# Optimization experiments

Hardware: AMD Instinct MI355X
Metric: run time of the kernel (lower is better)

## Reference

```python
import jax, jax.numpy as jnp
import numpy as np

B, S, N = 64, 32, 128            # batch, seq_len, padded nodes per graph
DV, DW, DH = 512, 300, 1024      # dim_v, dim_word, dim_hidden
CLS, T_CTRL, L = 1024, 12, 4     # cls_fc_dim, controller steps, stack_len
NQ, NA, NE, NATTR, M = 100, 28, 16, 1000, 6  # vocabs, edge cats, attrs, num modules
# module order: 0 NoOp, 1 Find(push), 2 Transform, 3 Filter, 4 And, 5 Describe

def _valid_mat():
    m = np.zeros((L, M), dtype=np.float32)
    for s in range(L):
        m[s, 0] = 1.0
        m[s, 1] = 1.0 if s < L - 1 else 0.0
        m[s, 2] = 1.0 if s >= 1 else 0.0
        m[s, 3] = 1.0 if s >= 1 else 0.0
        m[s, 4] = 1.0 if s >= 2 else 0.0
        m[s, 5] = 1.0 if s >= 1 else 0.0
    return jnp.asarray(m)

VALID_MAT = _valid_mat()

def setup_inputs() -> dict:
    key = jax.random.key(0)
    ks = jax.random.split(key, 24)
    nrm = lambda k, sh, sc: jax.random.normal(k, sh, jnp.float32) * sc
    inp = {}
    inp['questions'] = jax.random.randint(ks[0], (B, S), 0, NQ)
    inp['questions_len'] = jax.random.randint(ks[1], (B,), 8, S + 1)
    inp['conn'] = (jax.random.uniform(ks[2], (B, N, N)) < 0.2).astype(jnp.float32)
    inp['cat_mat'] = jax.random.randint(ks[3], (B, N, N), 0, NE)
    inp['v_idx'] = jax.random.randint(ks[4], (B, N), 0, NATTR)
    inp['attr_emb'] = nrm(ks[5], (NATTR, DV), 1.0 / np.sqrt(DV))
    inp['edge_cat_vectors'] = nrm(ks[6], (NE, DV), 1.0 / np.sqrt(DV))
    inp['enc_emb'] = nrm(ks[7], (NQ, DW), 1.0 / np.sqrt(DW))
    inp['Wx'] = nrm(ks[8], (DW, 4 * DH), 1.0 / np.sqrt(DW))
    inp['Wh'] = nrm(ks[9], (DH, 4 * DH), 1.0 / np.sqrt(DH))
    inp['b_lstm'] = jnp.zeros((4 * DH,), jnp.float32)
    inp['W_cq'] = nrm(ks[10], (2 * DH, DH), 1.0 / np.sqrt(2 * DH))
    inp['b_cq'] = jnp.zeros((DH,), jnp.float32)
    inp['W_mod'] = nrm(ks[11], (DH, M), 1.0 / np.sqrt(DH))
    inp['W_att'] = nrm(ks[12], (DH, DH), 1.0 / np.sqrt(DH))
    inp['W_q'] = nrm(ks[13], (DH, DV), np.sqrt(2.0 / DH))
    inp['b_q'] = jnp.zeros((DV,), jnp.float32)
    inp['W_find'] = nrm(ks[14], (DV, DV), 1.0 / np.sqrt(DV))
    inp['W_desc'] = nrm(ks[15], (DV, DV), 1.0 / np.sqrt(DV))
    inp['W_cls1'] = nrm(ks[16], (DV + DH, CLS), np.sqrt(2.0 / (DV + DH)))
    inp['b_cls1'] = jnp.zeros((CLS,), jnp.float32)
    inp['W_cls2'] = nrm(ks[17], (CLS, NA), np.sqrt(2.0 / CLS))
    inp['b_cls2'] = jnp.zeros((NA,), jnp.float32)
    return inp

def _read(st, p):
    return jnp.einsum('bnl,bl->bn', st, p)

def _write(st, p, a):
    pe = p[:, None, :]
    return a[:, :, None] * pe + st * (1.0 - pe)

def _ptr_fw(p):
    q = jnp.concatenate([jnp.zeros_like(p[:, :1]), p[:, :-1]], axis=1)
    return q.at[:, -1].add(p[:, -1])

def _ptr_bw(p):
    q = jnp.concatenate([p[:, 1:], jnp.zeros_like(p[:, :1])], axis=1)
    return q.at[:, 0].add(p[:, 0])

def reference(questions, questions_len, conn, cat_mat, v_idx, attr_emb,
              edge_cat_vectors, enc_emb, Wx, Wh, b_lstm, W_cq, b_cq, W_mod,
              W_att, W_q, b_q, W_find, W_desc, W_cls1, b_cls1, W_cls2, b_cls2):
    # ---- question encoder: embedding + LSTM over time-major sequence ----
    emb = enc_emb[questions].transpose(1, 0, 2)  # [S,B,DW]

    def lstm_step(carry, x):
        h, c = carry
        g = x @ Wx + h @ Wh + b_lstm
        i, f, gg, o = jnp.split(g, 4, axis=-1)
        c = jax.nn.sigmoid(f) * c + jax.nn.sigmoid(i) * jnp.tanh(gg)
        h = jax.nn.sigmoid(o) * jnp.tanh(c)
        return (h, c), h

    init = (jnp.zeros((B, DH), jnp.float32), jnp.zeros((B, DH), jnp.float32))
    _, outs = jax.lax.scan(lstm_step, init, emb)            # [S,B,DH]
    outs_b = outs.transpose(1, 0, 2)                         # [B,S,DH]
    q_hidden = outs_b[jnp.arange(B), questions_len - 1]      # last valid state

    mask = jnp.arange(S)[:, None] < questions_len[None, :]   # [S,B]
    feat = attr_emb[v_idx]                                   # [B,N,DV]
    bidx = jnp.arange(B)[:, None, None]

    att_stack = jnp.zeros((B, N, L), jnp.float32)
    stack_ptr = jnp.zeros((B, L), jnp.float32).at[:, 0].set(1.0)
    mem = jnp.zeros((B, DV), jnp.float32)
    c_ctrl = jnp.zeros((B, DH), jnp.float32)
    inv_sqrt_dv = 1.0 / np.sqrt(DV)

    for t in range(T_CTRL):
        # ---- controller step: module distribution + textual attention ----
        cq = jnp.tanh(jnp.concatenate([c_ctrl, q_hidden], axis=1) @ W_cq + b_cq)
        module_prob = jax.nn.softmax(cq @ W_mod, axis=-1)     # [B,M]
        al = jnp.einsum('sbh,bh->sb', outs, cq @ W_att)
        cv = jax.nn.softmax(jnp.where(mask, al, -1e9), axis=0)
        c_ctrl = jnp.einsum('sb,sbh->bh', cv, outs)
        c_i = jax.nn.relu(c_ctrl @ W_q + b_q)                 # [B,DV]

        # ---- validity masking of module distribution ----
        validity = jnp.round(stack_ptr @ VALID_MAT)           # [B,M]
        mp = module_prob * validity
        s = jnp.sum(mp, axis=1, keepdims=True)
        mp = mp / jnp.where(s > 0, s, 1.0)

        # ---- run every module, soft-average by module prob ----
        a_find = jax.nn.sigmoid(jnp.einsum('bnd,bd->bn', feat @ W_find, c_i) * inv_sqrt_dv)
        a_in = _read(att_stack, stack_ptr)
        # Transform: edge-category-weighted message passing on graph
        we = jax.nn.softmax(c_i @ edge_cat_vectors.T, axis=-1)   # [B,NE]
        ew = we[bidx, cat_mat] * conn                            # [B,N,N]
        a_trans = jnp.minimum(jnp.einsum('bij,bj->bi', ew, a_in), 1.0)
        p_fw = _ptr_fw(stack_ptr)
        p_bw = _ptr_bw(stack_ptr)
        a_prev = _read(att_stack, p_bw)
        pooled = jnp.einsum('bn,bnd->bd', a_in, feat) / (jnp.sum(a_in, 1, keepdims=True) + 1e-6)
        res = [
            (att_stack, stack_ptr, mem),                                  # NoOp
            (_write(att_stack, p_fw, a_find), p_fw, mem),                 # Find (push)
            (_write(att_stack, stack_ptr, a_trans), stack_ptr, mem),      # Transform
            (_write(att_stack, stack_ptr, a_in * a_find), stack_ptr, mem),# Filter
            (_write(att_stack, p_bw, jnp.minimum(a_prev, a_in)), p_bw, mem),  # And (pop)
            (att_stack, p_bw, pooled @ W_desc),                           # Describe
        ]
        att_stack = jnp.einsum('bm,mbnl->bnl', mp, jnp.stack([r[0] for r in res]))
        stack_ptr = jnp.einsum('bm,mbl->bl', mp, jnp.stack([r[1] for r in res]))
        mem = jnp.einsum('bm,mbd->bd', mp, jnp.stack([r[2] for r in res]))

    final = jnp.concatenate([mem, q_hidden], axis=1)
    h1 = jax.nn.relu(final @ W_cls1 + b_cls1)
    logits = h1 @ W_cls2 + b_cls2
    return logits
```

## Files before the change

kernel.cpp:

```cpp
#include <hip/hip_runtime.h>
#include <math.h>

#define B 64
#define S 32
#define NN 128
#define DV 512
#define DW 300
#define DH 1024
#define CLS 1024
#define T_CTRL 12
#define LL 4
#define NA 28
#define NE 16
#define MM 6

__device__ __forceinline__ float sigmoidf_(float x) { return 1.0f / (1.0f + expf(-x)); }

template<bool TRANS, class AF, class WF>
__device__ __forceinline__ void gemm_core(int kbeg, int Kc, AF loadA, WF loadW,
                                          float* part, int Cld, int orow) {
  __shared__ float Ast[2][64 * 36];
  __shared__ float Ws[2][32 * 64];
  const int tid = threadIdx.x;
  const int j0 = blockIdx.x * 64;
  const int ntiles = Kc >> 5;
  const int rg = tid & 15, cg = tid >> 4;
  float4 av[2], wv[2];

  auto fetch = [&](int kt) {
    #pragma unroll
    for (int i2 = 0; i2 < 2; ++i2) {
      int idx = tid + i2 * 256;
      av[i2] = loadA(idx >> 3, kt + (idx & 7) * 4);
    }
    #pragma unroll
    for (int i2 = 0; i2 < 2; ++i2) {
      int idx = tid + i2 * 256;
      if (!TRANS) wv[i2] = loadW(kt + (idx >> 4), j0 + (idx & 15) * 4);
      else        wv[i2] = loadW(j0 + (idx >> 3), kt + (idx & 7) * 4);
    }
  };
  auto commit = [&](int buf) {
    #pragma unroll
    for (int i2 = 0; i2 < 2; ++i2) {
      int idx = tid + i2 * 256;
      *(float4*)&Ast[buf][(idx >> 3) * 36 + (idx & 7) * 4] = av[i2];
    }
    #pragma unroll
    for (int i2 = 0; i2 < 2; ++i2) {
      int idx = tid + i2 * 256;
      if (!TRANS) {
        *(float4*)&Ws[buf][(idx >> 4) * 64 + (idx & 15) * 4] = wv[i2];
      } else {
        int jloc = idx >> 3, k4 = (idx & 7) * 4;
        Ws[buf][(k4 + 0) * 64 + jloc] = wv[i2].x;
        Ws[buf][(k4 + 1) * 64 + jloc] = wv[i2].y;
        Ws[buf][(k4 + 2) * 64 + jloc] = wv[i2].z;
        Ws[buf][(k4 + 3) * 64 + jloc] = wv[i2].w;
      }
    }
  };

  float acc[4][4] = {};
  fetch(kbeg);
  commit(0);
  __syncthreads();
  for (int i = 0; i < ntiles; ++i) {
    if (i + 1 < ntiles) fetch(kbeg + (i + 1) * 32);
    const float* As = &Ast[i & 1][0];
    const float* Wp = &Ws[i & 1][0];
    #pragma unroll
    for (int kq = 0; kq < 8; ++kq) {
      float4 a0 = *(const float4*)&As[(rg     ) * 36 + kq * 4];
      float4 a1 = *(const float4*)&As[(rg + 16) * 36 + kq * 4];
      float4 a2 = *(const float4*)&As[(rg + 32) * 36 + kq * 4];
      float4 a3 = *(const float4*)&As[(rg + 48) * 36 + kq * 4];
      float4 w0 = *(const float4*)&Wp[(kq * 4 + 0) * 64 + cg * 4];
      float4 w1 = *(const float4*)&Wp[(kq * 4 + 1) * 64 + cg * 4];
      float4 w2 = *(const float4*)&Wp[(kq * 4 + 2) * 64 + cg * 4];
      float4 w3 = *(const float4*)&Wp[(kq * 4 + 3) * 64 + cg * 4];
      #define STEP(m, AV) \
        acc[m][0]=fmaf(AV.x,w0.x,acc[m][0]); acc[m][1]=fmaf(AV.x,w0.y,acc[m][1]); \
        acc[m][2]=fmaf(AV.x,w0.z,acc[m][2]); acc[m][3]=fmaf(AV.x,w0.w,acc[m][3]); \
        acc[m][0]=fmaf(AV.y,w1.x,acc[m][0]); acc[m][1]=fmaf(AV.y,w1.y,acc[m][1]); \
        acc[m][2]=fmaf(AV.y,w1.z,acc[m][2]); acc[m][3]=fmaf(AV.y,w1.w,acc[m][3]); \
        acc[m][0]=fmaf(AV.z,w2.x,acc[m][0]); acc[m][1]=fmaf(AV.z,w2.y,acc[m][1]); \
        acc[m][2]=fmaf(AV.z,w2.z,acc[m][2]); acc[m][3]=fmaf(AV.z,w2.w,acc[m][3]); \
        acc[m][0]=fmaf(AV.w,w3.x,acc[m][0]); acc[m][1]=fmaf(AV.w,w3.y,acc[m][1]); \
        acc[m][2]=fmaf(AV.w,w3.z,acc[m][2]); acc[m][3]=fmaf(AV.w,w3.w,acc[m][3]);
      STEP(0, a0) STEP(1, a1) STEP(2, a2) STEP(3, a3)
      #undef STEP
    }
    if (i + 1 < ntiles) { __syncthreads(); commit((i + 1) & 1); __syncthreads(); }
  }
  float* op = part + (size_t)orow * 64 * Cld + j0 + cg * 4;
  #pragma unroll
  for (int m = 0; m < 4; ++m)
    *(float4*)&op[(size_t)(rg + 16 * m) * Cld] = make_float4(acc[m][0], acc[m][1], acc[m][2], acc[m][3]);
}

__global__ void init_kernel(float* c_lstm, float* c_ctrl, float* att_stack, float* mem, float* sptr) {
  int idx = blockIdx.x * 256 + threadIdx.x;
  if (idx < B * DH) { c_lstm[idx] = 0.f; c_ctrl[idx] = 0.f; }
  if (idx < B * NN * LL) att_stack[idx] = 0.f;
  if (idx < B * DV) mem[idx] = 0.f;
  if (idx < B * LL) sptr[idx] = ((idx & (LL - 1)) == 0) ? 1.f : 0.f;
}

__global__ void embq_kernel(const int* __restrict__ questions, const float* __restrict__ enc_emb,
                            float* __restrict__ embq) {
  int row = blockIdx.x;
  int t = row >> 6, b = row & 63;
  int qid = questions[b * S + t];
  int c = threadIdx.x;
  embq[(size_t)row * 320 + c] = (c < DW) ? enc_emb[(size_t)qid * DW + c] : 0.f;
}

__global__ __launch_bounds__(256) void xgemm_kernel(const float* __restrict__ embq,
                                                    const float* __restrict__ Wx,
                                                    float* __restrict__ X) {
  auto Al = [&](int r, int k) -> float4 {
    return *(const float4*)&embq[(size_t)(blockIdx.y * 64 + r) * 320 + k];
  };
  auto Wl = [&](int k, int j) -> float4 {
    if (k < 300) return *(const float4*)&Wx[(size_t)k * 4096 + j];
    return make_float4(0.f, 0.f, 0.f, 0.f);
  };
  gemm_core<false>(0, 320, Al, Wl, X, 4096, blockIdx.y);
}

__global__ __launch_bounds__(256) void f2_kernel(const float* __restrict__ attr_emb,
                                                 const float* __restrict__ W_find,
                                                 float* __restrict__ F2) {
  auto Al = [&](int r, int k) -> float4 {
    int gr = blockIdx.y * 64 + r;
    if (gr > 999) gr = 999;
    return *(const float4*)&attr_emb[(size_t)gr * 512 + k];
  };
  auto Wl = [&](int k, int j) -> float4 { return *(const float4*)&W_find[(size_t)k * 512 + j]; };
  gemm_core<false>(0, 512, Al, Wl, F2, 512, blockIdx.y);
}

__global__ __launch_bounds__(256) void lstm_gemm_kernel(const float* __restrict__ h_prev,
                                                        const float* __restrict__ Wh,
                                                        float* __restrict__ part) {
  auto Al = [&](int r, int k) -> float4 { return *(const float4*)&h_prev[(size_t)r * 1024 + k]; };
  auto Wl = [&](int k, int j) -> float4 { return *(const float4*)&Wh[(size_t)k * 4096 + j]; };
  gemm_core<false>(blockIdx.y * 128, 128, Al, Wl, part, 4096, blockIdx.y);
}

__global__ __launch_bounds__(256) void lstm_gate_kernel(const float* __restrict__ part, int SK,
                                                        const float* __restrict__ X, int t,
                                                        const float* __restrict__ b_lstm,
                                                        float* __restrict__ h_out, float* __restrict__ c_st) {
  int idx = blockIdx.x * 256 + threadIdx.x;
  int b = idx >> 10, j = idx & 1023;
  const float* xr = X + ((size_t)t * 64 + b) * 4096;
  float gi = xr[j], gf = xr[1024 + j], gg = xr[2048 + j], go = xr[3072 + j];
  const float* pb = part + (size_t)b * 4096;
  for (int c = 0; c < SK; ++c) {
    const float* p = pb + (size_t)c * 262144;
    gi += p[j]; gf += p[1024 + j]; gg += p[2048 + j]; go += p[3072 + j];
  }
  gi += b_lstm[j]; gf += b_lstm[1024 + j]; gg += b_lstm[2048 + j]; go += b_lstm[3072 + j];
  float c = sigmoidf_(gf) * c_st[idx] + sigmoidf_(gi) * tanhf(gg);
  h_out[idx] = sigmoidf_(go) * tanhf(c);
  c_st[idx] = c;
}

__global__ __launch_bounds__(256) void c1_kernel(const float* __restrict__ c_ctrl,
                                                 const float* __restrict__ outs, const int* __restrict__ qlen,
                                                 const float* __restrict__ W_cq, float* __restrict__ partA,
                                                 const float* __restrict__ partE, const float* __restrict__ mp,
                                                 float* __restrict__ mem, int do_epi) {
  if (blockIdx.x == 16) {
    if (!do_epi) return;
    int t0 = blockIdx.y * 256 + threadIdx.x;
    #pragma unroll
    for (int i = 0; i < 4; ++i) {
      int f4 = t0 + i * 2048;
      int b = f4 >> 7, j = (f4 & 127) * 4;
      const float* m = &mp[b * 6];
      float s04 = m[0] + m[1] + m[2] + m[3] + m[4];
      float4 s = make_float4(0.f, 0.f, 0.f, 0.f);
      for (int c = 0; c < 8; ++c) {
        float4 v = *(const float4*)&partE[(size_t)c * 32768 + b * 512 + j];
        s.x += v.x; s.y += v.y; s.z += v.z; s.w += v.w;
      }
      float4 o = *(const float4*)&mem[b * 512 + j];
      o.x = s04 * o.x + m[5] * s.x; o.y = s04 * o.y + m[5] * s.y;
      o.z = s04 * o.z + m[5] * s.z; o.w = s04 * o.w + m[5] * s.w;
      *(float4*)&mem[b * 512 + j] = o;
    }
    return;
  }
  auto Al = [&](int r, int k) -> float4 {
    if (k < 1024) return *(const float4*)&c_ctrl[r * 1024 + k];
    int tq = qlen[r] - 1;
    return *(const float4*)&outs[(size_t)tq * 65536 + r * 1024 + (k - 1024)];
  };
  auto Wl = [&](int k, int j) -> float4 { return *(const float4*)&W_cq[(size_t)k * 1024 + j]; };
  gemm_core<false>(blockIdx.y * 256, 256, Al, Wl, partA, 1024, blockIdx.y);
}

__global__ __launch_bounds__(256) void c2_kernel(const float* __restrict__ partA,
                                                 const float* __restrict__ b_cq,
                                                 const float* __restrict__ W_att,
                                                 const float* __restrict__ W_mod,
                                                 float* __restrict__ partB) {
  auto Al = [&](int r, int k) -> float4 {
    float4 s = *(const float4*)&b_cq[k];
    for (int c = 0; c < 8; ++c) {
      float4 v = *(const float4*)&partA[(size_t)c * 65536 + r * 1024 + k];
      s.x += v.x; s.y += v.y; s.z += v.z; s.w += v.w;
    }
    return make_float4(tanhf(s.x), tanhf(s.y), tanhf(s.z), tanhf(s.w));
  };
  auto Wl = [&](int k, int j) -> float4 {
    if (j < 1024) return *(const float4*)&W_att[(size_t)k * 1024 + j];
    float v[4];
    #pragma unroll
    for (int i = 0; i < 4; ++i) {
      int jj = j + i;
      v[i] = (jj < 1030) ? W_mod[(size_t)k * 6 + (jj - 1024)] : 0.f;
    }
    return make_float4(v[0], v[1], v[2], v[3]);
  };
  gemm_core<false>(blockIdx.y * 64, 64, Al, Wl, partB, 1088, blockIdx.y);
}

__global__ __launch_bounds__(256) void attn_kernel(const float* __restrict__ partB,
                                                   const float* __restrict__ outs,
                                                   const int* __restrict__ qlen,
                                                   float* __restrict__ c_ctrl) {
  int b = blockIdx.x >> 2, hq = blockIdx.x & 3;
  int tid = threadIdx.x;
  __shared__ float aw[DH];
  __shared__ float alv[S];
  __shared__ float cvs[S];
  {
    int c4 = tid * 4;
    float4 s = make_float4(0.f, 0.f, 0.f, 0.f);
    for (int c = 0; c < 16; ++c) {
      float4 v = *(const float4*)&partB[(size_t)c * 69632 + b * 1088 + c4];
      s.x += v.x; s.y += v.y; s.z += v.z; s.w += v.w;
    }
    *(float4*)&aw[c4] = s;
  }
  __syncthreads();
  {
    int wv = tid >> 6, lane = tid & 63;
    #pragma unroll
    for (int u = 0; u < 4; ++u) {
      int s2 = wv * 4 + u;
      const float4* orow = (const float4*)&outs[(size_t)s2 * 65536 + b * 1024];
      float pr = 0.f;
      #pragma unroll
      for (int q = 0; q < 4; ++q) {
        float4 f = orow[lane + 64 * q];
        float4 w = *(const float4*)&aw[(lane + 64 * q) * 4];
        pr += f.x * w.x + f.y * w.y + f.z * w.z + f.w * w.w;
      }
      #pragma unroll
      for (int off = 32; off > 0; off >>= 1) pr += __shfl_xor(pr, off);
      if (lane == 0) alv[s2] = pr;
    }
  }
  __syncthreads();
  if (tid < 64) {
    int len = qlen[b];
    float v = (tid < S && tid < len) ? alv[tid] : -1e9f;
    float mx = v;
    #pragma unroll
    for (int off = 32; off > 0; off >>= 1) mx = fmaxf(mx, __shfl_xor(mx, off));
    float e = (tid < S && tid < len) ? expf(v - mx) : 0.f;
    float sm = e;
    #pragma unroll
    for (int off = 32; off > 0; off >>= 1) sm += __shfl_xor(sm, off);
    if (tid < S) cvs[tid] = e / sm;
  }
  __syncthreads();
  {
    int h = hq * 256 + tid;
    float a = 0.f;
    #pragma unroll 8
    for (int s2 = 0; s2 < S; ++s2)
      a = fmaf(cvs[s2], outs[(size_t)s2 * 65536 + b * 1024 + h], a);
    c_ctrl[b * 1024 + h] = a;
  }
}

__global__ __launch_bounds__(256) void c4_kernel(const float* __restrict__ c_ctrl,
                                                 const float* __restrict__ W_q,
                                                 float* __restrict__ partC) {
  auto Al = [&](int r, int k) -> float4 { return *(const float4*)&c_ctrl[r * 1024 + k]; };
  auto Wl = [&](int k, int j) -> float4 { return *(const float4*)&W_q[(size_t)k * 512 + j]; };
  gemm_core<false>(blockIdx.y * 64, 64, Al, Wl, partC, 512, blockIdx.y);
}

__global__ __launch_bounds__(256) void prep_kernel(const float* __restrict__ partC,
                                                   const float* __restrict__ partB,
                                                   const float* __restrict__ b_q,
                                                   const float* __restrict__ edge_cat,
                                                   const float* __restrict__ sptr_in,
                                                   const float* __restrict__ att_stack,
                                                   float* __restrict__ c_i, float* __restrict__ we,
                                                   float* __restrict__ mp, float* __restrict__ spv,
                                                   float* __restrict__ ain, float* __restrict__ aw4,
                                                   float* __restrict__ asum) {
  int b = blockIdx.x, tid = threadIdx.x;
  __shared__ float ci[512];
  __shared__ float lds[64];
  for (int col = tid; col < 512; col += 256) {
    float s = b_q[col];
    for (int c = 0; c < 16; ++c) s += partC[(size_t)c * 32768 + b * 512 + col];
    s = fmaxf(s, 0.f);
    ci[col] = s;
    c_i[b * 512 + col] = s;
  }
  if (tid < MM) {
    float s = 0.f;
    for (int c = 0; c < 16; ++c) s += partB[(size_t)c * 69632 + b * 1088 + 1024 + tid];
    lds[16 + tid] = s;
  }
  __syncthreads();
  {
    int wv = tid >> 6, lane = tid & 63;
    for (int e = wv; e < NE; e += 4) {
      const float* er = &edge_cat[(size_t)e * 512];
      float p = 0.f;
      #pragma unroll
      for (int q = 0; q < 8; ++q) p = fmaf(ci[lane + 64 * q], er[lane + 64 * q], p);
      #pragma unroll
      for (int off = 32; off > 0; off >>= 1) p += __shfl_xor(p, off);
      if (lane == 0) lds[e] = p;
    }
  }
  __syncthreads();
  if (tid == 0) {
    float mx = lds[0];
    for (int e = 1; e < NE; ++e) mx = fmaxf(mx, lds[e]);
    float sm = 0.f, ex[NE];
    for (int e = 0; e < NE; ++e) { ex[e] = expf(lds[e] - mx); sm += ex[e]; }
    for (int e = 0; e < NE; ++e) we[b * NE + e] = ex[e] / sm;
    float mx2 = lds[16];
    for (int m = 1; m < MM; ++m) mx2 = fmaxf(mx2, lds[16 + m]);
    float e6[MM], sm2 = 0.f;
    for (int m = 0; m < MM; ++m) { e6[m] = expf(lds[16 + m] - mx2); sm2 += e6[m]; }
    float p0 = sptr_in[b * 4 + 0], p1 = sptr_in[b * 4 + 1];
    float p2 = sptr_in[b * 4 + 2], p3 = sptr_in[b * 4 + 3];
    float sp[12];
    sp[0] = p0; sp[1] = p1; sp[2] = p2; sp[3] = p3;
    sp[4] = 0.f;      sp[5] = p0; sp[6] = p1; sp[7] = p2 + p3;
    sp[8] = p0 + p1;  sp[9] = p2; sp[10] = p3; sp[11] = 0.f;
    for (int i = 0; i < 12; ++i) { spv[b * 12 + i] = sp[i]; lds[22 + i] = sp[i]; }
    float val[MM];
    val[0] = rintf(p0 + p1 + p2 + p3);
    val[1] = rintf(p0 + p1 + p2);
    val[2] = rintf(p1 + p2 + p3);
    val[3] = val[2];
    val[4] = rintf(p2 + p3);
    val[5] = val[2];
    float mpv[MM], ssum = 0.f;
    #pragma unroll
    for (int m = 0; m < MM; ++m) { mpv[m] = (e6[m] / sm2) * val[m]; ssum += mpv[m]; }
    float inv = (ssum > 0.f) ? 1.f / ssum : 1.f;
    #pragma unroll
    for (int m = 0; m < MM; ++m) mp[b * MM + m] = mpv[m] * inv;
  }
  __syncthreads();
  if (tid < 128) {
    float4 st = *(const float4*)&att_stack[(b * NN + tid) * LL];
    float ainv = st.x * lds[22] + st.y * lds[23] + st.z * lds[24] + st.w * lds[25];
    float ap   = st.x * lds[30] + st.y * lds[31] + st.z * lds[32] + st.w * lds[33];
    ain[b * NN + tid] = ainv;
    aw4[b * NN + tid] = fminf(ap, ainv);
    float t2 = ainv;
    #pragma unroll
    for (int off = 32; off > 0; off >>= 1) t2 += __shfl_xor(t2, off);
    if ((tid & 63) == 0) lds[40 + (tid >> 6)] = t2;
  }
  __syncthreads();
  if (tid == 0) asum[b] = lds[40] + lds[41] + 1e-6f;
}

__global__ __launch_bounds__(256) void stackf_kernel(const int* __restrict__ v_idx,
                                                     const float* __restrict__ attr_emb,
                                                     const float* __restrict__ F2,
                                                     const float* __restrict__ c_i,
                                                     const float* __restrict__ we,
                                                     const int* __restrict__ cat_mat,
                                                     const float* __restrict__ conn,
                                                     const float* __restrict__ ain,
                                                     const float* __restrict__ asum,
                                                     float* __restrict__ afind,
                                                     float* __restrict__ atr,
                                                     float* __restrict__ pooled) {
  int job = blockIdx.x, tid = threadIdx.x;
  __shared__ float lds[192];
  if (job < 2048) {
    int gw = job * 4 + (tid >> 6);
    int b = gw >> 7, n = gw & 127, lane = tid & 63;
    int vid = v_idx[b * NN + n];
    const float4* fp = (const float4*)&F2[(size_t)vid * DV];
    const float4* up = (const float4*)&c_i[(size_t)b * DV];
    float pr = 0.f;
    #pragma unroll
    for (int q = 0; q < 2; ++q) {
      float4 f = fp[lane + 64 * q], u = up[lane + 64 * q];
      pr += f.x * u.x + f.y * u.y + f.z * u.z + f.w * u.w;
    }
    #pragma unroll
    for (int off = 32; off > 0; off >>= 1) pr += __shfl_xor(pr, off);
    if (lane == 0) afind[b * NN + n] = sigmoidf_(pr * 0.04419417382415922f);
  } else if (job < 2560) {
    int j2 = job - 2048;
    int b = j2 >> 3, ig = j2 & 7;
    if (tid < 128) lds[tid] = ain[b * NN + tid];
    else if (tid < 144) lds[tid] = we[b * NE + tid - 128];
    __syncthreads();
    int i = ig * 16 + (tid >> 4);
    const int* crow = &cat_mat[((size_t)b * NN + i) * NN];
    const float* nrow = &conn[((size_t)b * NN + i) * NN];
    float a = 0.f;
    #pragma unroll
    for (int q = 0; q < 8; ++q) {
      int j = (tid & 15) + 16 * q;
      a = fmaf(lds[128 + crow[j]] * nrow[j], lds[j], a);
    }
    a += __shfl_xor(a, 1); a += __shfl_xor(a, 2); a += __shfl_xor(a, 4); a += __shfl_xor(a, 8);
    if ((tid & 15) == 0) atr[b * NN + i] = fminf(a, 1.f);
  } else {
    int j3 = job - 2560;
    int b = j3 >> 1, d = (j3 & 1) * 256 + tid;
    int* vidL = (int*)&lds[128];
    if (tid < 128) { lds[tid] = ain[b * NN + tid]; vidL[tid] = v_idx[b * NN + tid]; }
    __syncthreads();
    float a = 0.f;
    #pragma unroll 4
    for (int n = 0; n < NN; ++n)
      a = fmaf(lds[n], attr_emb[(size_t)vidL[n] * DV + d], a);
    pooled[b * DV + d] = a / asum[b];
  }
}

__global__ __launch_bounds__(256) void c7u_kernel(const float* __restrict__ pooled,
                                                  const float* __restrict__ W_desc,
                                                  float* __restrict__ partE,
                                                  const float* __restrict__ spv,
                                                  const float* __restrict__ mp,
                                                  const float* __restrict__ afind,
                                                  const float* __restrict__ ain,
                                                  const float* __restrict__ atr,
                                                  const float* __restrict__ aw4,
                                                  float* __restrict__ att_stack,
                                                  float* __restrict__ sptr) {
  int tid = threadIdx.x;
  if (blockIdx.y < 8) {
    auto Al = [&](int r, int k) -> float4 { return *(const float4*)&pooled[r * 512 + k]; };
    auto Wl = [&](int k, int j) -> float4 { return *(const float4*)&W_desc[(size_t)k * 512 + j]; };
    gemm_core<false>(blockIdx.y * 64, 64, Al, Wl, partE, 512, blockIdx.y);
    return;
  }
  int b = (blockIdx.y - 8) * 8 + blockIdx.x;
  __shared__ float sp[12], smp[MM];
  if (tid < 12) sp[tid] = spv[b * 12 + tid];
  else if (tid < 12 + MM) smp[tid - 12] = mp[b * MM + (tid - 12)];
  __syncthreads();
  #pragma unroll
  for (int i = 0; i < 2; ++i) {
    int e = tid + i * 256;
    int n = e >> 2, l = e & 3;
    float st = att_stack[(b * NN + n) * LL + l];
    float keep = smp[0] + smp[5] + smp[1] * (1.f - sp[4 + l]) + (smp[2] + smp[3]) * (1.f - sp[l])
               + smp[4] * (1.f - sp[8 + l]);
    float add = sp[4 + l] * smp[1] * afind[b * NN + n]
              + sp[l] * (smp[2] * atr[b * NN + n] + smp[3] * ain[b * NN + n] * afind[b * NN + n])
              + sp[8 + l] * smp[4] * aw4[b * NN + n];
    att_stack[(b * NN + n) * LL + l] = keep * st + add;
  }
  if (tid < LL)
    sptr[b * LL + tid] = (smp[0] + smp[2] + smp[3]) * sp[tid] + smp[1] * sp[4 + tid]
                       + (smp[4] + smp[5]) * sp[8 + tid];
}

__global__ __launch_bounds__(256) void cl1_kernel(const float* __restrict__ partE,
                                                  const float* __restrict__ mp,
                                                  const float* __restrict__ mem,
                                                  const float* __restrict__ outs,
                                                  const int* __restrict__ qlen,
                                                  const float* __restrict__ W_cls1,
                                                  float* __restrict__ partH) {
  auto Al = [&](int r, int k) -> float4 {
    if (k < 512) {
      float4 s = make_float4(0.f, 0.f, 0.f, 0.f);
      for (int c = 0; c < 8; ++c) {
        float4 v = *(const float4*)&partE[(size_t)c * 32768 + r * 512 + k];
        s.x += v.x; s.y += v.y; s.z += v.z; s.w += v.w;
      }
      const float* m = &mp[r * 6];
      float s04 = m[0] + m[1] + m[2] + m[3] + m[4];
      float4 o = *(const float4*)&mem[r * 512 + k];
      return make_float4(s04 * o.x + m[5] * s.x, s04 * o.y + m[5] * s.y,
                         s04 * o.z + m[5] * s.z, s04 * o.w + m[5] * s.w);
    }
    int tq = qlen[r] - 1;
    return *(const float4*)&outs[(size_t)tq * 65536 + r * 1024 + (k - 512)];
  };
  auto Wl = [&](int k, int j) -> float4 { return *(const float4*)&W_cls1[(size_t)k * 1024 + j]; };
  gemm_core<false>(blockIdx.y * 192, 192, Al, Wl, partH, 1024, blockIdx.y);
}

__global__ __launch_bounds__(256) void cl2_kernel(const float* __restrict__ partH,
                                                  const float* __restrict__ b_cls1,
                                                  const float* __restrict__ W_cls2,
                                                  float* __restrict__ partJ) {
  auto Al = [&](int r, int k) -> float4 {
    float4 s = *(const float4*)&b_cls1[k];
    for (int c = 0; c < 8; ++c) {
      float4 v = *(const float4*)&partH[(size_t)c * 65536 + r * 1024 + k];
      s.x += v.x; s.y += v.y; s.z += v.z; s.w += v.w;
    }
    return make_float4(fmaxf(s.x, 0.f), fmaxf(s.y, 0.f), fmaxf(s.z, 0.f), fmaxf(s.w, 0.f));
  };
  auto Wl = [&](int k, int j) -> float4 {
    float v[4];
    #pragma unroll
    for (int i = 0; i < 4; ++i) { int jj = j + i; v[i] = (jj < NA) ? W_cls2[(size_t)k * NA + jj] : 0.f; }
    return make_float4(v[0], v[1], v[2], v[3]);
  };
  gemm_core<false>(blockIdx.y * 128, 128, Al, Wl, partJ, 64, blockIdx.y);
}

__global__ void cl3_kernel(const float* __restrict__ partJ, const float* __restrict__ b_cls2,
                           float* __restrict__ logits) {
  int idx = blockIdx.x * 256 + threadIdx.x;
  if (idx >= B * NA) return;
  int r = idx / NA, j = idx - r * NA;
  float s = b_cls2[j];
  for (int c = 0; c < 8; ++c) s += partJ[(size_t)c * 4096 + r * 64 + j];
  logits[idx] = s;
}

extern "C" void kernel_launch(void* const* d_in, const int* in_sizes, int n_in,
                              void* d_out, int out_size, void* d_ws, size_t ws_size,
                              hipStream_t stream) {
  const int*   questions = (const int*)d_in[0];
  const int*   qlen      = (const int*)d_in[1];
  const float* conn      = (const float*)d_in[2];
  const int*   cat_mat   = (const int*)d_in[3];
  const int*   v_idx     = (const int*)d_in[4];
  const float* attr_emb  = (const float*)d_in[5];
  const float* edge_cat  = (const float*)d_in[6];
  const float* enc_emb   = (const float*)d_in[7];
  const float* Wx        = (const float*)d_in[8];
  const float* Wh        = (const float*)d_in[9];
  const float* b_lstm    = (const float*)d_in[10];
  const float* W_cq      = (const float*)d_in[11];
  const float* b_cq      = (const float*)d_in[12];
  const float* W_mod     = (const float*)d_in[13];
  const float* W_att     = (const float*)d_in[14];
  const float* W_q       = (const float*)d_in[15];
  const float* b_q       = (const float*)d_in[16];
  const float* W_find    = (const float*)d_in[17];
  const float* W_desc    = (const float*)d_in[18];
  const float* W_cls1    = (const float*)d_in[19];
  const float* b_cls1    = (const float*)d_in[20];
  const float* W_cls2    = (const float*)d_in[21];
  const float* b_cls2    = (const float*)d_in[22];
  float* logits = (float*)d_out;

  float* w = (float*)d_ws;
  size_t off = 0;
  float* outs      = w + off; off += (size_t)S * B * DH;
  float* embq      = w + off; off += (size_t)S * B * 320;
  float* X         = w + off; off += (size_t)S * B * 4096;
  float* F2        = w + off; off += 1024 * 512;
  float* share     = w + off; off += 2457600;
  float* partE     = w + off; off += 262144;
  float* partH     = w + off; off += 524288;
  float* partJ     = w + off; off += 32768;
  float* c_ctrl    = w + off; off += B * DH;
  float* c_lstm    = w + off; off += B * DH;
  float* ci_buf    = w + off; off += B * DV;
  float* we_buf    = w + off; off += B * NE;
  float* mp_buf    = w + off; off += B * MM;
  float* spv_buf   = w + off; off += B * 12;
  float* ain_buf   = w + off; off += B * NN;
  float* aw4_buf   = w + off; off += B * NN;
  float* afind_buf = w + off; off += B * NN;
  float* atr_buf   = w + off; off += B * NN;
  float* asum_buf  = w + off; off += B;
  float* att_stack = w + off; off += B * NN * LL;
  float* sptr_buf  = w + off; off += B * LL;
  float* mem       = w + off; off += B * DV;
  float* pooled    = w + off; off += B * DV;

  float* partLSTM = share;
  float* partA = share;
  float* partB = share + 524288;
  float* partC = share + 1638400;

  init_kernel<<<256, 256, 0, stream>>>(c_lstm, c_ctrl, att_stack, mem, sptr_buf);
  embq_kernel<<<S * B, 320, 0, stream>>>(questions, enc_emb, embq);
  xgemm_kernel<<<dim3(64, 32), 256, 0, stream>>>(embq, Wx, X);
  f2_kernel<<<dim3(8, 16), 256, 0, stream>>>(attr_emb, W_find, F2);

  lstm_gate_kernel<<<(B * DH) / 256, 256, 0, stream>>>(partLSTM, 0, X, 0, b_lstm, outs, c_lstm);
  for (int t = 1; t < S; ++t) {
    lstm_gemm_kernel<<<dim3(64, 8), 256, 0, stream>>>(outs + (size_t)(t - 1) * B * DH, Wh, partLSTM);
    lstm_gate_kernel<<<(B * DH) / 256, 256, 0, stream>>>(partLSTM, 8, X, t, b_lstm,
                                                         outs + (size_t)t * B * DH, c_lstm);
  }

  for (int it = 0; it < T_CTRL; ++it) {
    c1_kernel<<<dim3(17, 8), 256, 0, stream>>>(c_ctrl, outs, qlen, W_cq, partA,
                                               partE, mp_buf, mem, it > 0 ? 1 : 0);
    c2_kernel<<<dim3(17, 16), 256, 0, stream>>>(partA, b_cq, W_att, W_mod, partB);
    attn_kernel<<<256, 256, 0, stream>>>(partB, outs, qlen, c_ctrl);
    c4_kernel<<<dim3(8, 16), 256, 0, stream>>>(c_ctrl, W_q, partC);
    prep_kernel<<<64, 256, 0, stream>>>(partC, partB, b_q, edge_cat, sptr_buf, att_stack,
                                        ci_buf, we_buf, mp_buf, spv_buf, ain_buf, aw4_buf, asum_buf);
    stackf_kernel<<<2688, 256, 0, stream>>>(v_idx, attr_emb, F2, ci_buf, we_buf, cat_mat, conn,
                                            ain_buf, asum_buf, afind_buf, atr_buf, pooled);
    c7u_kernel<<<dim3(8, 16), 256, 0, stream>>>(pooled, W_desc, partE, spv_buf, mp_buf,
                                                afind_buf, ain_buf, atr_buf, aw4_buf,
                                                att_stack, sptr_buf);
  }

  cl1_kernel<<<dim3(16, 8), 256, 0, stream>>>(partE, mp_buf, mem, outs, qlen, W_cls1, partH);
  cl2_kernel<<<dim3(1, 8), 256, 0, stream>>>(partH, b_cls1, W_cls2, partJ);
  cl3_kernel<<<7, 256, 0, stream>>>(partJ, b_cls2, logits);
}
```

Before: 1.494 ms.

## Fuse LSTM gate into recurrent GEMM via atomic last-block-done counters

Merges the per-step LSTM gate kernel into the split-K recurrent GEMM kernel. Each block bumps an atomic counter per (column group, batch quarter) after a release fence, and the last of the 32 contributing blocks applies the gate reduction and cell update with float4 loads. This removes 31 kernel launches and one round trip through global memory for the partial sums. In exchange it adds atomics, fences and a serial tail on the last-arriving block, and relies on monotonically increasing counters being exact across steps.

```diff
diff --git a/kernel.cpp b/kernel.cpp
--- a/kernel.cpp
+++ b/kernel.cpp
@@ -99,12 +99,14 @@
     *(float4*)&op[(size_t)(rg + 16 * m) * Cld] = make_float4(acc[m][0], acc[m][1], acc[m][2], acc[m][3]);
 }
 
-__global__ void init_kernel(float* c_lstm, float* c_ctrl, float* att_stack, float* mem, float* sptr) {
+__global__ void init_kernel(float* c_lstm, float* c_ctrl, float* att_stack, float* mem, float* sptr,
+                            int* cnt) {
   int idx = blockIdx.x * 256 + threadIdx.x;
   if (idx < B * DH) { c_lstm[idx] = 0.f; c_ctrl[idx] = 0.f; }
   if (idx < B * NN * LL) att_stack[idx] = 0.f;
   if (idx < B * DV) mem[idx] = 0.f;
   if (idx < B * LL) sptr[idx] = ((idx & (LL - 1)) == 0) ? 1.f : 0.f;
+  if (idx < 1024) cnt[idx] = 0;
 }
 
 __global__ void embq_kernel(const int* __restrict__ questions, const float* __restrict__ enc_emb,
@@ -141,29 +143,86 @@
   gemm_core<false>(0, 512, Al, Wl, F2, 512, blockIdx.y);
 }
 
-__global__ __launch_bounds__(256) void lstm_gemm_kernel(const float* __restrict__ h_prev,
+__global__ __launch_bounds__(256) void lstm_step_kernel(const float* __restrict__ h_prev,
                                                         const float* __restrict__ Wh,
-                                                        float* __restrict__ part) {
+                                                        float* __restrict__ part,
+                                                        const float* __restrict__ X, int t,
+                                                        const float* __restrict__ b_lstm,
+                                                        float* __restrict__ h_out,
+                                                        float* __restrict__ c_st,
+                                                        int* __restrict__ cnt) {
   auto Al = [&](int r, int k) -> float4 { return *(const float4*)&h_prev[(size_t)r * 1024 + k]; };
   auto Wl = [&](int k, int j) -> float4 { return *(const float4*)&Wh[(size_t)k * 4096 + j]; };
   gemm_core<false>(blockIdx.y * 128, 128, Al, Wl, part, 4096, blockIdx.y);
-}
-
-__global__ __launch_bounds__(256) void lstm_gate_kernel(const float* __restrict__ part, int SK,
-                                                        const float* __restrict__ X, int t,
-                                                        const float* __restrict__ b_lstm,
-                                                        float* __restrict__ h_out, float* __restrict__ c_st) {
+
+  __shared__ int sel[4];
+  const int tid = threadIdx.x;
+  const int g = blockIdx.x & 15;
+  __syncthreads();
+  if (tid < 4) {
+    __builtin_amdgcn_fence(__ATOMIC_RELEASE, "agent");
+    int old = atomicAdd(&cnt[(g * 4 + tid) * 16], 1);
+    sel[tid] = (old == 32 * t - 1) ? 1 : 0;
+  }
+  __syncthreads();
+  if (sel[0] | sel[1] | sel[2] | sel[3]) {
+    if (tid == 0) __builtin_amdgcn_fence(__ATOMIC_ACQUIRE, "agent");
+    __syncthreads();
+    #pragma unroll
+    for (int q = 0; q < 4; ++q) {
+      if (!sel[q]) continue;
+      int b = q * 16 + (tid >> 4);
+      int j = g * 64 + (tid & 15) * 4;
+      const float* xr = X + ((size_t)t * 64 + b) * 4096;
+      float4 gi = *(const float4*)&xr[j];
+      float4 gf = *(const float4*)&xr[1024 + j];
+      float4 gg = *(const float4*)&xr[2048 + j];
+      float4 go = *(const float4*)&xr[3072 + j];
+      for (int c = 0; c < 8; ++c) {
+        const float* p = part + (size_t)c * 262144 + b * 4096;
+        float4 v;
+        v = *(const float4*)&p[j];        gi.x += v.x; gi.y += v.y; gi.z += v.z; gi.w += v.w;
+        v = *(const float4*)&p[1024 + j]; gf.x += v.x; gf.y += v.y; gf.z += v.z; gf.w += v.w;
+        v = *(const float4*)&p[2048 + j]; gg.x += v.x; gg.y += v.y; gg.z += v.z; gg.w += v.w;
+        v = *(const float4*)&p[3072 + j]; go.x += v.x; go.y += v.y; go.z += v.z; go.w += v.w;
+      }
+      float4 bi = *(const float4*)&b_lstm[j];
+      float4 bf = *(const float4*)&b_lstm[1024 + j];
+      float4 bg = *(const float4*)&b_lstm[2048 + j];
+      float4 bo = *(const float4*)&b_lstm[3072 + j];
+      gi.x += bi.x; gi.y += bi.y; gi.z += bi.z; gi.w += bi.w;
+      gf.x += bf.x; gf.y += bf.y; gf.z += bf.z; gf.w += bf.w;
+      gg.x += bg.x; gg.y += bg.y; gg.z += bg.z; gg.w += bg.w;
+      go.x += bo.x; go.y += bo.y; go.z += bo.z; go.w += bo.w;
+      int idx = b * 1024 + j;
+      float4 cv = *(const float4*)&c_st[idx];
+      float4 cn, hn;
+      cn.x = sigmoidf_(gf.x) * cv.x + sigmoidf_(gi.x) * tanhf(gg.x);
+      cn.y = sigmoidf_(gf.y) * cv.y + sigmoidf_(gi.y) * tanhf(gg.y);
+      cn.z = sigmoidf_(gf.z) * cv.z + sigmoidf_(gi.z) * tanhf(gg.z);
+      cn.w = sigmoidf_(gf.w) * cv.w + sigmoidf_(gi.w) * tanhf(gg.w);
+      hn.x = sigmoidf_(go.x) * tanhf(cn.x);
+      hn.y = sigmoidf_(go.y) * tanhf(cn.y);
+      hn.z = sigmoidf_(go.z) * tanhf(cn.z);
+      hn.w = sigmoidf_(go.w) * tanhf(cn.w);
+      *(float4*)&c_st[idx] = cn;
+      *(float4*)&h_out[idx] = hn;
+    }
+  }
+}
+
+__global__ __launch_bounds__(256) void lstm_gate0_kernel(const float* __restrict__ X,
+                                                         const float* __restrict__ b_lstm,
+                                                         float* __restrict__ h_out,
+                                                         float* __restrict__ c_st) {
   int idx = blockIdx.x * 256 + threadIdx.x;
   int b = idx >> 10, j = idx & 1023;
-  const float* xr = X + ((size_t)t * 64 + b) * 4096;
-  float gi = xr[j], gf = xr[1024 + j], gg = xr[2048 + j], go = xr[3072 + j];
-  const float* pb = part + (size_t)b * 4096;
-  for (int c = 0; c < SK; ++c) {
-    const float* p = pb + (size_t)c * 262144;
-    gi += p[j]; gf += p[1024 + j]; gg += p[2048 + j]; go += p[3072 + j];
-  }
-  gi += b_lstm[j]; gf += b_lstm[1024 + j]; gg += b_lstm[2048 + j]; go += b_lstm[3072 + j];
-  float c = sigmoidf_(gf) * c_st[idx] + sigmoidf_(gi) * tanhf(gg);
+  const float* xr = X + (size_t)b * 4096;
+  float gi = xr[j] + b_lstm[j];
+  float gf = xr[1024 + j] + b_lstm[1024 + j];
+  float gg = xr[2048 + j] + b_lstm[2048 + j];
+  float go = xr[3072 + j] + b_lstm[3072 + j];
+  float c = sigmoidf_(gi) * tanhf(gg);
   h_out[idx] = sigmoidf_(go) * tanhf(c);
   c_st[idx] = c;
 }
@@ -595,22 +654,23 @@
   float* sptr_buf  = w + off; off += B * LL;
   float* mem       = w + off; off += B * DV;
   float* pooled    = w + off; off += B * DV;
+  int*   cnt       = (int*)(w + off); off += 1024;
 
   float* partLSTM = share;
   float* partA = share;
   float* partB = share + 524288;
   float* partC = share + 1638400;
 
-  init_kernel<<<256, 256, 0, stream>>>(c_lstm, c_ctrl, att_stack, mem, sptr_buf);
+  init_kernel<<<256, 256, 0, stream>>>(c_lstm, c_ctrl, att_stack, mem, sptr_buf, cnt);
   embq_kernel<<<S * B, 320, 0, stream>>>(questions, enc_emb, embq);
   xgemm_kernel<<<dim3(64, 32), 256, 0, stream>>>(embq, Wx, X);
   f2_kernel<<<dim3(8, 16), 256, 0, stream>>>(attr_emb, W_find, F2);
 
-  lstm_gate_kernel<<<(B * DH) / 256, 256, 0, stream>>>(partLSTM, 0, X, 0, b_lstm, outs, c_lstm);
+  lstm_gate0_kernel<<<(B * DH) / 256, 256, 0, stream>>>(X, b_lstm, outs, c_lstm);
   for (int t = 1; t < S; ++t) {
-    lstm_gemm_kernel<<<dim3(64, 8), 256, 0, stream>>>(outs + (size_t)(t - 1) * B * DH, Wh, partLSTM);
-    lstm_gate_kernel<<<(B * DH) / 256, 256, 0, stream>>>(partLSTM, 8, X, t, b_lstm,
-                                                         outs + (size_t)t * B * DH, c_lstm);
+    lstm_step_kernel<<<dim3(64, 8), 256, 0, stream>>>(outs + (size_t)(t - 1) * B * DH, Wh,
+                                                      partLSTM, X, t, b_lstm,
+                                                      outs + (size_t)t * B * DH, c_lstm, cnt);
   }
 
   for (int it = 0; it < T_CTRL; ++it) {
```

Measured after the change: 2.014 ms. 1.35x slower.
